# Kernel optimization log

Hardware: AMD Instinct MI355X
Metric: run time of the kernel (lower is better)

Reference implementation:

```python
import jax, jax.numpy as jnp
import numpy as np

# init_kwargs: conv_k=1, scale=1
CONV_K = 1
P = 3 - CONV_K          # scale == 1 branch
PAD_X = (P + 1) // 2    # 1 (applied before: top/left)
PAD_Y = P // 2          # 1 (applied after: bottom/right)


def setup_inputs() -> dict:
    key = jax.random.key(0)
    x = jax.random.normal(key, (16, 256, 128, 128), dtype=jnp.float32)
    return {"x": x}


def reference(x):
    # Fixed FIR kernel f = [1,3,3,1]; norm_fir_k -> 2D outer product, normalized.
    f1 = jnp.array([1.0, 3.0, 3.0, 1.0], dtype=x.dtype)
    k = jnp.outer(f1, f1)
    k = k / jnp.sum(k)
    # upfirdn2d performs true convolution (kernel flipped); symmetric here but kept for fidelity.
    k = jnp.flip(k, (0, 1))
    C = x.shape[1]
    w = jnp.broadcast_to(k[None, None], (C, 1, 4, 4))  # depthwise filter
    out = jax.lax.conv_general_dilated(
        x, w,
        window_strides=(1, 1),
        padding=((PAD_X, PAD_Y), (PAD_X, PAD_Y)),
        feature_group_count=C,
        dimension_numbers=("NCHW", "OIHW", "NCHW"),
    )
    # out: [16, 256, 127, 127] = H + padX + padY - 4 + 1
    return out
```

## Files before the change

kernel.cpp:

```cpp
#include <hip/hip_runtime.h>


#define IW 128
#define IH 128
#define OW 127
#define OH 127

typedef float f4u __attribute__((ext_vector_type(4), aligned(4)));

__global__ __launch_bounds__(128)
void upfirdn2d_blur_v3(const float4* __restrict__ x, float* __restrict__ out) {
    const int tid = threadIdx.x;
    const int c   = tid & 31;
    const int s   = tid >> 5;
    const int img = blockIdx.x;

    const float4* __restrict__ in4 = x + (size_t)img * (IH * IW / 4);
    float*        __restrict__ o   = out + (size_t)img * (OH * OW);

    const float mL   = (c > 0)  ? 1.0f : 0.0f;
    const float mR   = (c < 31) ? 1.0f : 0.0f;
    const bool  edge = (c == 31);
    const int lm1 = (tid - 1) & 63;
    const int lp1 = (tid + 1) & 63;

    float* const obase = o + 4 * c - (edge ? 1 : 0);

    auto hrow = [&](int r) -> float4 {
        const float4 v = in4[r * (IW / 4) + c];
        const float l  = mL * __shfl(v.w, lm1, 64);
        const float r0 = mR * __shfl(v.x, lp1, 64);
        const float r1 = mR * __shfl(v.y, lp1, 64);
        float4 h;
        h.x = l   + 3.0f * (v.x + v.y) + v.z;
        h.y = v.x + 3.0f * (v.y + v.z) + v.w;
        h.z = v.y + 3.0f * (v.z + v.w) + r0;
        h.w = v.z + 3.0f * (v.w + r0)  + r1;
        return h;
    };

    const int y0 = 32 * s;

    float4 hm1 = hrow(y0 > 0 ? y0 - 1 : 0);
    const float mTop = (y0 > 0) ? 1.0f : 0.0f;
    hm1.x *= mTop; hm1.y *= mTop; hm1.z *= mTop; hm1.w *= mTop;
    float4 h0 = hrow(y0);
    float4 h1 = hrow(y0 + 1);

    #pragma unroll 4
    for (int i = 0; i < 32; ++i) {
        const int y  = y0 + i;
        const int r2 = y + 2;
        const float m2 = (r2 < IH) ? 1.0f : 0.0f;
        float4 h2 = hrow(r2 < IH ? r2 : IH - 1);
        h2.x *= m2; h2.y *= m2; h2.z *= m2; h2.w *= m2;

        if (y < OH) {
            float4 t;
            t.x = (hm1.x + 3.0f * (h0.x + h1.x) + h2.x) * 0.015625f;
            t.y = (hm1.y + 3.0f * (h0.y + h1.y) + h2.y) * 0.015625f;
            t.z = (hm1.z + 3.0f * (h0.z + h1.z) + h2.z) * 0.015625f;
            t.w = (hm1.w + 3.0f * (h0.w + h1.w) + h2.w) * 0.015625f;

            const float tw = __shfl(t.w, lm1, 64);
            f4u sv;
            sv[0] = edge ? tw  : t.x;
            sv[1] = edge ? t.x : t.y;
            sv[2] = edge ? t.y : t.z;
            sv[3] = edge ? t.z : t.w;
            *(f4u*)(obase + y * OW) = sv;
        }
        hm1 = h0; h0 = h1; h1 = h2;
    }
}

extern "C" void kernel_launch(void* const* d_in, const int* in_sizes, int n_in,
                              void* d_out, int out_size, void* d_ws, size_t ws_size,
                              hipStream_t stream) {
    const float4* x = (const float4*)d_in[0];
    float* out = (float*)d_out;
    const int n_imgs = 16 * 256;
    hipLaunchKernelGGL(upfirdn2d_blur_v3, dim3(n_imgs), dim3(128), 0, stream,
                       x, out);
}
```

Measured before the change: 465.1 us.

## Prefetch all input rows into registers and use 8 row-strips per image

Doubles the block to 256 threads so each 32-lane group handles 16 output rows instead of 32. All 19 needed input rows are loaded into a register array up front and the loop is fully unrolled, so loads are issued together instead of one per iteration. This aims to raise memory-level parallelism and hide global load latency on a bandwidth-bound blur. The cost is higher register pressure and more redundant halo row loads per image.

```diff
diff --git a/kernel.cpp b/kernel.cpp
--- a/kernel.cpp
+++ b/kernel.cpp
@@ -5,15 +5,17 @@
 #define IH 128
 #define OW 127
 #define OH 127
+#define NPF 19
 
 typedef float f4u __attribute__((ext_vector_type(4), aligned(4)));
 
-__global__ __launch_bounds__(128)
-void upfirdn2d_blur_v3(const float4* __restrict__ x, float* __restrict__ out) {
-    const int tid = threadIdx.x;
-    const int c   = tid & 31;
-    const int s   = tid >> 5;
-    const int img = blockIdx.x;
+__global__ __launch_bounds__(256)
+void upfirdn2d_blur_v5(const float4* __restrict__ x, float* __restrict__ out) {
+    const int tid  = threadIdx.x;
+    const int lane = tid & 63;
+    const int c    = lane & 31;
+    const int s    = tid >> 5;
+    const int img  = blockIdx.x;
 
     const float4* __restrict__ in4 = x + (size_t)img * (IH * IW / 4);
     float*        __restrict__ o   = out + (size_t)img * (OH * OW);
@@ -21,40 +23,44 @@
     const float mL   = (c > 0)  ? 1.0f : 0.0f;
     const float mR   = (c < 31) ? 1.0f : 0.0f;
     const bool  edge = (c == 31);
-    const int lm1 = (tid - 1) & 63;
-    const int lp1 = (tid + 1) & 63;
+    const int lm1 = (lane - 1) & 63;
+    const int lp1 = (lane + 1) & 63;
 
     float* const obase = o + 4 * c - (edge ? 1 : 0);
 
-    auto hrow = [&](int r) -> float4 {
-        const float4 v = in4[r * (IW / 4) + c];
+    const int y0 = 16 * s;
+
+    float4 pf[NPF];
+    #pragma unroll
+    for (int j = 0; j < NPF; ++j) {
+        int r = y0 - 1 + j;
+        r = r < 0 ? 0 : (r > IH - 1 ? IH - 1 : r);
+        pf[j] = in4[r * (IW / 4) + c];
+    }
+
+    auto hof = [&](const float4 v, const float m) -> float4 {
         const float l  = mL * __shfl(v.w, lm1, 64);
         const float r0 = mR * __shfl(v.x, lp1, 64);
         const float r1 = mR * __shfl(v.y, lp1, 64);
         float4 h;
-        h.x = l   + 3.0f * (v.x + v.y) + v.z;
-        h.y = v.x + 3.0f * (v.y + v.z) + v.w;
-        h.z = v.y + 3.0f * (v.z + v.w) + r0;
-        h.w = v.z + 3.0f * (v.w + r0)  + r1;
+        h.x = (l   + 3.0f * (v.x + v.y) + v.z) * m;
+        h.y = (v.x + 3.0f * (v.y + v.z) + v.w) * m;
+        h.z = (v.y + 3.0f * (v.z + v.w) + r0)  * m;
+        h.w = (v.z + 3.0f * (v.w + r0)  + r1)  * m;
         return h;
     };
 
-    const int y0 = 32 * s;
+    float4 hm1 = hof(pf[0], (s == 0) ? 0.0f : 1.0f);
+    float4 h0  = hof(pf[1], 1.0f);
+    float4 h1  = hof(pf[2], 1.0f);
 
-    float4 hm1 = hrow(y0 > 0 ? y0 - 1 : 0);
-    const float mTop = (y0 > 0) ? 1.0f : 0.0f;
-    hm1.x *= mTop; hm1.y *= mTop; hm1.z *= mTop; hm1.w *= mTop;
-    float4 h0 = hrow(y0);
-    float4 h1 = hrow(y0 + 1);
+    #pragma unroll
+    for (int i = 0; i < 16; ++i) {
+        const int j2 = i + 3;
+        const float m2 = (y0 + i + 2 < IH) ? 1.0f : 0.0f;
+        float4 h2 = hof(pf[j2], m2);
 
-    #pragma unroll 4
-    for (int i = 0; i < 32; ++i) {
-        const int y  = y0 + i;
-        const int r2 = y + 2;
-        const float m2 = (r2 < IH) ? 1.0f : 0.0f;
-        float4 h2 = hrow(r2 < IH ? r2 : IH - 1);
-        h2.x *= m2; h2.y *= m2; h2.z *= m2; h2.w *= m2;
-
+        const int y = y0 + i;
         if (y < OH) {
             float4 t;
             t.x = (hm1.x + 3.0f * (h0.x + h1.x) + h2.x) * 0.015625f;
@@ -80,6 +86,6 @@
     const float4* x = (const float4*)d_in[0];
     float* out = (float*)d_out;
     const int n_imgs = 16 * 256;
-    hipLaunchKernelGGL(upfirdn2d_blur_v3, dim3(n_imgs), dim3(128), 0, stream,
+    hipLaunchKernelGGL(upfirdn2d_blur_v5, dim3(n_imgs), dim3(256), 0, stream,
                        x, out);
 }
```

Result: faster. 437.4 us (-5.9%).
